# Optimization experiments

Hardware: AMD Instinct MI355X
Metric: run time of the kernel (lower is better)

Reference implementation:

```python
import jax, jax.numpy as jnp
import numpy as np

DIM = 2048
NUM_HEADS = 16
HEAD_DIM = DIM // NUM_HEADS  # 128
HIDDEN = HEAD_DIM * NUM_HEADS  # 2048


def setup_inputs() -> dict:
    key = jax.random.key(0)
    k1, k2, k3 = jax.random.split(key, 3)
    x = jax.random.normal(k1, (2, 4096, DIM), dtype=jnp.float32)
    # match torch init: gates.weight ~ N(0, dim**-0.5), output.weight ~ N(0, hidden**-0.5)
    Wg = jax.random.normal(k2, (NUM_HEADS + 3 * HIDDEN, DIM), dtype=jnp.float32) * DIM ** -0.5
    bg = jnp.zeros((NUM_HEADS + 3 * HIDDEN,), dtype=jnp.float32)
    Wo = jax.random.normal(k3, (DIM, HIDDEN), dtype=jnp.float32) * HIDDEN ** -0.5
    bo = jnp.zeros((DIM,), dtype=jnp.float32)
    return {"x": x, "Wg": Wg, "bg": bg, "Wo": Wo, "bo": bo}


def _combine(a, b):
    # linear recurrence c_t = f_t * c_{t-1} + u_t as an associative op
    fa, ua = a
    fb, ub = b
    return fa * fb, fb * ua + ub


def reference(x, Wg, bg, Wo, bo):
    # x: [B, T, dim]
    g = jnp.einsum('btd,gd->btg', x, Wg) + bg  # [B, T, H + 3*hidden]
    f = jax.nn.sigmoid(g[..., :NUM_HEADS])  # [B, T, H]
    i = jax.nn.sigmoid(g[..., NUM_HEADS:NUM_HEADS + HIDDEN])
    t = jnp.tanh(g[..., NUM_HEADS + HIDDEN:NUM_HEADS + 2 * HIDDEN])
    o = g[..., NUM_HEADS + 2 * HIDDEN:]
    f = jnp.repeat(f, HEAD_DIM, axis=-1)  # tied forget gate per head -> [B, T, hidden]
    update = i * t
    # scan over time axis (axis=1)
    _, c = jax.lax.associative_scan(_combine, (f, update), axis=1)
    h = o * jnp.tanh(c)
    return jnp.einsum('bth,dh->btd', h, Wo) + bo
```

## Files before the change

kernel.cpp:

```cpp
#include <hip/hip_runtime.h>
#include <hip/hip_bf16.h>

#define DIM 2048
#define NHEADS 16
#define HEAD_DIM 128
#define HIDDEN 2048
#define SEQ 4096
#define BATCH 2
#define BT (BATCH * SEQ)
#define NSEG 64
#define SEGLEN (SEQ / NSEG)
#define N_GATE (3 * HIDDEN)

typedef __bf16 bf16_t;
typedef __bf16 bf16x8 __attribute__((ext_vector_type(8)));
typedef __bf16 bf16x4_t __attribute__((ext_vector_type(4)));
typedef float f32x4 __attribute__((ext_vector_type(4)));

__device__ __forceinline__ void gload_lds16(const void* g, void* l) {
  __builtin_amdgcn_global_load_lds(
      (const __attribute__((address_space(1))) void*)g,
      (__attribute__((address_space(3))) void*)l, 16, 0, 0);
}

#define MEMFENCE asm volatile("" ::: "memory")
#define BAR do { MEMFENCE; __builtin_amdgcn_s_barrier(); MEMFENCE; } while (0)
#define VMCNT(n) asm volatile("s_waitcnt vmcnt(" #n ")" ::: "memory")

__global__ void cvt_f32_bf16(const float* __restrict__ src, bf16_t* __restrict__ dst, int n4) {
  int i = blockIdx.x * blockDim.x + threadIdx.x;
  if (i >= n4) return;
  float4 v = reinterpret_cast<const float4*>(src)[i];
  bf16x4_t o;
  o[0] = (bf16_t)v.x; o[1] = (bf16_t)v.y; o[2] = (bf16_t)v.z; o[3] = (bf16_t)v.w;
  reinterpret_cast<bf16x4_t*>(dst)[i] = o;
}

__global__ void fgate_kernel(const float* __restrict__ x, const float* __restrict__ Wg,
                             const float* __restrict__ bg, float* __restrict__ fout) {
  int idx = blockIdx.x * 256 + threadIdx.x;
  int bt = idx >> 4, h = idx & 15;
  const float* xr = x + (size_t)bt * DIM;
  const float* wr = Wg + (size_t)h * DIM;
  float acc = 0.f;
  for (int k = 0; k < DIM; k += 4) {
    float4 xv = *reinterpret_cast<const float4*>(xr + k);
    float4 wv = *reinterpret_cast<const float4*>(wr + k);
    acc = fmaf(xv.x, wv.x, acc);
    acc = fmaf(xv.y, wv.y, acc);
    acc = fmaf(xv.z, wv.z, acc);
    acc = fmaf(xv.w, wv.w, acc);
  }
  acc += bg[h];
  fout[idx] = 1.f / (1.f + expf(-acc));
}


__device__ __forceinline__ void stageA(const bf16_t* __restrict__ G, int brow, int kc,
                                       bf16_t* Aslot, int q, int wid, int lane) {
  const int rr = q * 64 + wid * 8;
  const int grow = brow + (wid >> 2) * 128 + q * 32 + (wid & 3) * 8 + (lane >> 3);
  const int gcol = kc + (((lane & 7) ^ (lane >> 3)) << 3);
  gload_lds16(G + (size_t)grow * 2048 + gcol, Aslot + (size_t)rr * 64);
}

__device__ __forceinline__ void stageB(const bf16_t* __restrict__ G, int bcol, int kc,
                                       bf16_t* Bslot, int j, int wid, int lane) {
  const int rr = (j >> 1) * 128 + (j & 1) * 64 + wid * 8;
  const int grow = bcol + rr + (lane >> 3);
  const int gcol = kc + (((lane & 7) ^ (lane >> 3)) << 3);
  gload_lds16(G + (size_t)grow * 2048 + gcol, Bslot + (size_t)rr * 64);
}

#define FRAG8(ptr, row, fo) (*reinterpret_cast<const bf16x8*>(&(ptr)[(size_t)(row) * 64 + (fo)]))

template <int MODE>
__global__ __launch_bounds__(512, 1)
void gemm256(const bf16_t* __restrict__ A, const bf16_t* __restrict__ B,
             const float* __restrict__ bias,
             bf16_t* __restrict__ Oi, bf16_t* __restrict__ Ot, bf16_t* __restrict__ Oo,
             float* __restrict__ Of, int tiles_n) {
  __shared__ __align__(16) bf16_t As[2][256 * 64];
  __shared__ __align__(16) bf16_t Bs[2][256 * 64];
  constexpr int KT = 32;

  const int tid = threadIdx.x;
  const int wid = tid >> 6, lane = tid & 63;
  const int nwg = gridDim.x, bid = blockIdx.x;
  const int swz = (bid & 7) * (nwg >> 3) + (bid >> 3);
  const int tm = swz / tiles_n, tn = swz - tm * tiles_n;
  const int brow = tm * 256, bcol = tn * 256;
  const int wm = wid >> 2, wn = wid & 3;
  const int rl = lane & 15, qw = lane >> 4;
  const int fo0 = ((qw ^ (rl & 7)) << 3);
  const int fo1 = fo0 ^ 32;
  const int brr = (wn >> 1) * 128 + (wn & 1) * 64;

  f32x4 acc[8][4] = {};

#pragma unroll
  for (int j = 0; j < 4; ++j) stageB(B, bcol, 0, &Bs[0][0], j, wid, lane);
#pragma unroll
  for (int qq = 0; qq < 4; ++qq) stageA(A, brow, 0, &As[0][0], qq, wid, lane);
#pragma unroll
  for (int qq = 0; qq < 3; ++qq) stageA(A, brow, 64, &As[1][0], qq, wid, lane);
  VMCNT(3);
  BAR;

  for (int t = 0; t < KT; ++t) {
    const int s = t & 1, ns = s ^ 1;
    const int kc1 = (t + 1) * 64, kc2 = (t + 2) * 64;
    const bool st1 = (t + 1) < KT, st2 = (t + 2) < KT;
    const bf16_t* Ar = &As[s][0];
    const bf16_t* Br = &Bs[s][0];
    bf16x8 bfr[2][4], af[2][2];

#define MFMA16(p)                                                                         \
  __builtin_amdgcn_s_setprio(1);                                                          \
  _Pragma("unroll")                                                                       \
  for (int mi = 0; mi < 2; ++mi)                                                          \
    _Pragma("unroll")                                                                     \
    for (int ni = 0; ni < 4; ++ni)                                                        \
      acc[(p)*2 + mi][ni] =                                                               \
          __builtin_amdgcn_mfma_f32_16x16x32_bf16(af[0][mi], bfr[0][ni], acc[(p)*2 + mi][ni], 0, 0, 0); \
  _Pragma("unroll")                                                                       \
  for (int mi = 0; mi < 2; ++mi)                                                          \
    _Pragma("unroll")                                                                     \
    for (int ni = 0; ni < 4; ++ni)                                                        \
      acc[(p)*2 + mi][ni] =                                                               \
          __builtin_amdgcn_mfma_f32_16x16x32_bf16(af[1][mi], bfr[1][ni], acc[(p)*2 + mi][ni], 0, 0, 0); \
  __builtin_amdgcn_s_setprio(0)

#pragma unroll
    for (int ni = 0; ni < 4; ++ni) {
      bfr[0][ni] = FRAG8(Br, brr + ni * 16 + rl, fo0);
      bfr[1][ni] = FRAG8(Br, brr + ni * 16 + rl, fo1);
    }
#pragma unroll
    for (int mi = 0; mi < 2; ++mi) {
      af[0][mi] = FRAG8(Ar, 0 * 64 + wm * 32 + mi * 16 + rl, fo0);
      af[1][mi] = FRAG8(Ar, 0 * 64 + wm * 32 + mi * 16 + rl, fo1);
    }
    if (st1) { stageB(B, bcol, kc1, &Bs[ns][0], 0, wid, lane);
               stageB(B, bcol, kc1, &Bs[ns][0], 1, wid, lane); }
    BAR;
    MFMA16(0);

#pragma unroll
    for (int mi = 0; mi < 2; ++mi) {
      af[0][mi] = FRAG8(Ar, 1 * 64 + wm * 32 + mi * 16 + rl, fo0);
      af[1][mi] = FRAG8(Ar, 1 * 64 + wm * 32 + mi * 16 + rl, fo1);
    }
    if (st1) { stageB(B, bcol, kc1, &Bs[ns][0], 2, wid, lane);
               stageB(B, bcol, kc1, &Bs[ns][0], 3, wid, lane); }
    if (t < KT - 1) { VMCNT(4); } else { VMCNT(0); }
    BAR;
    MFMA16(1);

#pragma unroll
    for (int mi = 0; mi < 2; ++mi) {
      af[0][mi] = FRAG8(Ar, 2 * 64 + wm * 32 + mi * 16 + rl, fo0);
      af[1][mi] = FRAG8(Ar, 2 * 64 + wm * 32 + mi * 16 + rl, fo1);
    }
    if (st2) { stageA(A, brow, kc2, &As[s][0], 0, wid, lane);
               stageA(A, brow, kc2, &As[s][0], 1, wid, lane); }
    BAR;
    MFMA16(2);

#pragma unroll
    for (int mi = 0; mi < 2; ++mi) {
      af[0][mi] = FRAG8(Ar, 3 * 64 + wm * 32 + mi * 16 + rl, fo0);
      af[1][mi] = FRAG8(Ar, 3 * 64 + wm * 32 + mi * 16 + rl, fo1);
    }
    if (st2) stageA(A, brow, kc2, &As[s][0], 2, wid, lane);
    if (st1) stageA(A, brow, kc1, &As[ns][0], 3, wid, lane);
    if (t < KT - 2) { VMCNT(4); }
    else if (t == KT - 2) { VMCNT(1); }
    BAR;
    MFMA16(3);
#undef MFMA16
  }

  const int crow0 = brow + wm * 128;
  const int ccol0 = bcol + wn * 64;
  if (MODE == 0) {
    const int section = bcol >> 11;
    bf16_t* dst = (section == 0) ? Oi : ((section == 1) ? Ot : Oo);
#pragma unroll
    for (int mi = 0; mi < 8; ++mi)
#pragma unroll
      for (int ni = 0; ni < 4; ++ni) {
        int gcol = ccol0 + ni * 16 + (lane & 15);
        int col = gcol & 2047;
        float bv = bias[gcol];
#pragma unroll
        for (int qq = 0; qq < 4; ++qq) {
          int row = crow0 + mi * 16 + (lane >> 4) * 4 + qq;
          float v = acc[mi][ni][qq] + bv;
          float aout;
          if (section == 0)      aout = 1.f / (1.f + __expf(-v));
          else if (section == 1) aout = tanhf(v);
          else                   aout = v;
          dst[(size_t)row * HIDDEN + col] = (bf16_t)aout;
        }
      }
  } else {
#pragma unroll
    for (int mi = 0; mi < 8; ++mi)
#pragma unroll
      for (int ni = 0; ni < 4; ++ni) {
        int col = ccol0 + ni * 16 + (lane & 15);
        float bv = bias[col];
#pragma unroll
        for (int qq = 0; qq < 4; ++qq) {
          int row = crow0 + mi * 16 + (lane >> 4) * 4 + qq;
          Of[(size_t)row * DIM + col] = acc[mi][ni][qq] + bv;
        }
      }
  }
}

__global__ void scan_pass1(const float* __restrict__ fg, const bf16_t* __restrict__ gi,
                           const bf16_t* __restrict__ gt, float* __restrict__ cend,
                           float* __restrict__ pseg) {
  int bx = blockIdx.x;
  int chblk = bx & 7, seg = (bx >> 3) & 63, b = bx >> 9;
  int ch = chblk * 256 + threadIdx.x;
  int head = ch >> 7;
  float c = 0.f, P = 1.f;
  size_t t0 = (size_t)b * SEQ + (size_t)seg * SEGLEN;
  for (int tt = 0; tt < SEGLEN; ++tt) {
    size_t bt = t0 + tt;
    float f = fg[bt * NHEADS + head];
    float iv = (float)gi[bt * HIDDEN + ch];
    float tv = (float)gt[bt * HIDDEN + ch];
    c = fmaf(f, c, iv * tv);
    P *= f;
  }
  size_t o = ((size_t)b * NSEG + seg) * HIDDEN + ch;
  cend[o] = c;
  pseg[o] = P;
}

__global__ void scan_pass2(const float* __restrict__ cend, const float* __restrict__ pseg,
                           float* __restrict__ cin) {
  int idx = blockIdx.x * 256 + threadIdx.x;
  int b = idx >> 11, ch = idx & 2047;
  float C = 0.f;
  for (int s = 0; s < NSEG; ++s) {
    size_t o = ((size_t)b * NSEG + s) * HIDDEN + ch;
    cin[o] = C;
    C = cend[o] + pseg[o] * C;
  }
}

__global__ void scan_pass3(const float* __restrict__ fg, const bf16_t* __restrict__ gi,
                           const bf16_t* __restrict__ gt, const bf16_t* __restrict__ go,
                           const float* __restrict__ cin, bf16_t* __restrict__ h) {
  int bx = blockIdx.x;
  int chblk = bx & 7, seg = (bx >> 3) & 63, b = bx >> 9;
  int ch = chblk * 256 + threadIdx.x;
  int head = ch >> 7;
  float c = cin[((size_t)b * NSEG + seg) * HIDDEN + ch];
  size_t t0 = (size_t)b * SEQ + (size_t)seg * SEGLEN;
  for (int tt = 0; tt < SEGLEN; ++tt) {
    size_t bt = t0 + tt;
    float f = fg[bt * NHEADS + head];
    float iv = (float)gi[bt * HIDDEN + ch];
    float tv = (float)gt[bt * HIDDEN + ch];
    c = fmaf(f, c, iv * tv);
    float hv = (float)go[bt * HIDDEN + ch] * tanhf(c);
    h[bt * HIDDEN + ch] = (bf16_t)hv;
  }
}

extern "C" void kernel_launch(void* const* d_in, const int* in_sizes, int n_in,
                              void* d_out, int out_size, void* d_ws, size_t ws_size,
                              hipStream_t stream) {
  const float* x  = (const float*)d_in[0];
  const float* Wg = (const float*)d_in[1];
  const float* bg = (const float*)d_in[2];
  const float* Wo = (const float*)d_in[3];
  const float* bo = (const float*)d_in[4];
  float* out = (float*)d_out;

  char* ws = (char*)d_ws;
  size_t off = 0;
  auto alloc = [&](size_t bytes) -> void* {
    void* p = ws + off;
    off += (bytes + 255) & ~(size_t)255;
    return p;
  };
  bf16_t* xb   = (bf16_t*)alloc((size_t)BT * DIM * 2);
  bf16_t* wgb  = (bf16_t*)alloc((size_t)N_GATE * DIM * 2);
  bf16_t* wob  = (bf16_t*)alloc((size_t)DIM * HIDDEN * 2);
  float*  fg   = (float*)alloc((size_t)BT * NHEADS * 4);
  bf16_t* gi   = (bf16_t*)alloc((size_t)BT * HIDDEN * 2);
  bf16_t* gt   = (bf16_t*)alloc((size_t)BT * HIDDEN * 2);
  bf16_t* go   = (bf16_t*)alloc((size_t)BT * HIDDEN * 2);
  bf16_t* hbuf = (bf16_t*)alloc((size_t)BT * HIDDEN * 2);
  float*  cend = (float*)alloc((size_t)BATCH * NSEG * HIDDEN * 4);
  float*  pseg = (float*)alloc((size_t)BATCH * NSEG * HIDDEN * 4);
  float*  cin  = (float*)alloc((size_t)BATCH * NSEG * HIDDEN * 4);
  (void)ws_size; (void)in_sizes; (void)n_in; (void)out_size;

  {
    int n4 = BT * DIM / 4;
    cvt_f32_bf16<<<(n4 + 255) / 256, 256, 0, stream>>>(x, xb, n4);
  }
  {
    int n4 = N_GATE * DIM / 4;
    cvt_f32_bf16<<<(n4 + 255) / 256, 256, 0, stream>>>(Wg + (size_t)NHEADS * DIM, wgb, n4);
  }
  {
    int n4 = DIM * HIDDEN / 4;
    cvt_f32_bf16<<<(n4 + 255) / 256, 256, 0, stream>>>(Wo, wob, n4);
  }

  fgate_kernel<<<(BT * NHEADS) / 256, 256, 0, stream>>>(x, Wg, bg, fg);

  gemm256<0><<<768, 512, 0, stream>>>(xb, wgb, bg + NHEADS, gi, gt, go, nullptr, 24);

  scan_pass1<<<BATCH * NSEG * (HIDDEN / 256), 256, 0, stream>>>(fg, gi, gt, cend, pseg);
  scan_pass2<<<BATCH * HIDDEN / 256, 256, 0, stream>>>(cend, pseg, cin);
  scan_pass3<<<BATCH * NSEG * (HIDDEN / 256), 256, 0, stream>>>(fg, gi, gt, go, cin, hbuf);

  gemm256<1><<<256, 512, 0, stream>>>(hbuf, wob, bo, nullptr, nullptr, nullptr, out, 8);
}
```

Measured before the change: 498.8 us.

## Use 4 waves per 256x256 GEMM tile with 128x128 per-wave subtiles

The 256x256 bf16 GEMM block drops from 8 waves to 4, and each wave now computes a 128x128 output subtile (8x8 MFMA fragments) instead of 128x64. This roughly doubles per-wave register reuse of A/B fragments from LDS and halves LDS read traffic per MFMA. Global-to-LDS staging is rewritten for 256 threads with more loads per thread and adjusted vmcnt waits. The cost is 256 accumulator registers per lane and less latency hiding from fewer waves per CU, which risks spills or stalls.

```diff
diff --git a/kernel.cpp b/kernel.cpp
--- a/kernel.cpp
+++ b/kernel.cpp
@@ -56,26 +56,18 @@
 }
 
 
-__device__ __forceinline__ void stageA(const bf16_t* __restrict__ G, int brow, int kc,
-                                       bf16_t* Aslot, int q, int wid, int lane) {
-  const int rr = q * 64 + wid * 8;
-  const int grow = brow + (wid >> 2) * 128 + q * 32 + (wid & 3) * 8 + (lane >> 3);
-  const int gcol = kc + (((lane & 7) ^ (lane >> 3)) << 3);
-  gload_lds16(G + (size_t)grow * 2048 + gcol, Aslot + (size_t)rr * 64);
-}
-
-__device__ __forceinline__ void stageB(const bf16_t* __restrict__ G, int bcol, int kc,
-                                       bf16_t* Bslot, int j, int wid, int lane) {
-  const int rr = (j >> 1) * 128 + (j & 1) * 64 + wid * 8;
-  const int grow = bcol + rr + (lane >> 3);
-  const int gcol = kc + (((lane & 7) ^ (lane >> 3)) << 3);
-  gload_lds16(G + (size_t)grow * 2048 + gcol, Bslot + (size_t)rr * 64);
+__device__ __forceinline__ void stage_u(const bf16_t* __restrict__ G, int grow0, int kc,
+                                        bf16_t* region, int u, int tid) {
+  const int row = u * 32 + (tid >> 3);
+  const int c = (tid & 7) ^ ((tid >> 3) & 7);
+  gload_lds16(G + (size_t)(grow0 + row) * 2048 + kc + c * 8,
+              region + (size_t)(u * 32 + (tid >> 6) * 8) * 64);
 }
 
 #define FRAG8(ptr, row, fo) (*reinterpret_cast<const bf16x8*>(&(ptr)[(size_t)(row) * 64 + (fo)]))
 
 template <int MODE>
-__global__ __launch_bounds__(512, 1)
+__global__ __launch_bounds__(256, 1)
 void gemm256(const bf16_t* __restrict__ A, const bf16_t* __restrict__ B,
              const float* __restrict__ bias,
              bf16_t* __restrict__ Oi, bf16_t* __restrict__ Ot, bf16_t* __restrict__ Oo,
@@ -90,21 +82,24 @@
   const int swz = (bid & 7) * (nwg >> 3) + (bid >> 3);
   const int tm = swz / tiles_n, tn = swz - tm * tiles_n;
   const int brow = tm * 256, bcol = tn * 256;
-  const int wm = wid >> 2, wn = wid & 3;
+  const int wm = wid >> 1, wn = wid & 1;
   const int rl = lane & 15, qw = lane >> 4;
   const int fo0 = ((qw ^ (rl & 7)) << 3);
   const int fo1 = fo0 ^ 32;
-  const int brr = (wn >> 1) * 128 + (wn & 1) * 64;
-
-  f32x4 acc[8][4] = {};
-
-#pragma unroll
-  for (int j = 0; j < 4; ++j) stageB(B, bcol, 0, &Bs[0][0], j, wid, lane);
-#pragma unroll
-  for (int qq = 0; qq < 4; ++qq) stageA(A, brow, 0, &As[0][0], qq, wid, lane);
-#pragma unroll
-  for (int qq = 0; qq < 3; ++qq) stageA(A, brow, 64, &As[1][0], qq, wid, lane);
-  VMCNT(3);
+
+  f32x4 acc[8][8] = {};
+
+#pragma unroll
+  for (int u = 0; u < 8; ++u) stage_u(B, bcol, 0, &Bs[0][0], u, tid);
+#pragma unroll
+  for (int u = 0; u < 8; ++u) stage_u(A, brow, 0, &As[0][0], u, tid);
+  stage_u(A, brow, 64, &As[1][0], 0, tid);
+  stage_u(A, brow, 64, &As[1][0], 1, tid);
+  stage_u(A, brow, 64, &As[1][0], 4, tid);
+  stage_u(A, brow, 64, &As[1][0], 5, tid);
+  stage_u(A, brow, 64, &As[1][0], 2, tid);
+  stage_u(A, brow, 64, &As[1][0], 6, tid);
+  VMCNT(6);
   BAR;
 
   for (int t = 0; t < KT; ++t) {
@@ -113,90 +108,100 @@
     const bool st1 = (t + 1) < KT, st2 = (t + 2) < KT;
     const bf16_t* Ar = &As[s][0];
     const bf16_t* Br = &Bs[s][0];
-    bf16x8 bfr[2][4], af[2][2];
-
-#define MFMA16(p)                                                                         \
+    bf16x8 bfr[2][8], af[2][2];
+
+#define MFMA32(p)                                                                         \
   __builtin_amdgcn_s_setprio(1);                                                          \
   _Pragma("unroll")                                                                       \
   for (int mi = 0; mi < 2; ++mi)                                                          \
     _Pragma("unroll")                                                                     \
-    for (int ni = 0; ni < 4; ++ni)                                                        \
-      acc[(p)*2 + mi][ni] =                                                               \
-          __builtin_amdgcn_mfma_f32_16x16x32_bf16(af[0][mi], bfr[0][ni], acc[(p)*2 + mi][ni], 0, 0, 0); \
+    for (int nj = 0; nj < 8; ++nj)                                                        \
+      acc[(p)*2 + mi][nj] =                                                               \
+          __builtin_amdgcn_mfma_f32_16x16x32_bf16(af[0][mi], bfr[0][nj], acc[(p)*2 + mi][nj], 0, 0, 0); \
   _Pragma("unroll")                                                                       \
   for (int mi = 0; mi < 2; ++mi)                                                          \
     _Pragma("unroll")                                                                     \
-    for (int ni = 0; ni < 4; ++ni)                                                        \
-      acc[(p)*2 + mi][ni] =                                                               \
-          __builtin_amdgcn_mfma_f32_16x16x32_bf16(af[1][mi], bfr[1][ni], acc[(p)*2 + mi][ni], 0, 0, 0); \
+    for (int nj = 0; nj < 8; ++nj)                                                        \
+      acc[(p)*2 + mi][nj] =                                                               \
+          __builtin_amdgcn_mfma_f32_16x16x32_bf16(af[1][mi], bfr[1][nj], acc[(p)*2 + mi][nj], 0, 0, 0); \
   __builtin_amdgcn_s_setprio(0)
 
 #pragma unroll
-    for (int ni = 0; ni < 4; ++ni) {
-      bfr[0][ni] = FRAG8(Br, brr + ni * 16 + rl, fo0);
-      bfr[1][ni] = FRAG8(Br, brr + ni * 16 + rl, fo1);
+    for (int nj = 0; nj < 8; ++nj) {
+      bfr[0][nj] = FRAG8(Br, wn * 128 + nj * 16 + rl, fo0);
+      bfr[1][nj] = FRAG8(Br, wn * 128 + nj * 16 + rl, fo1);
     }
 #pragma unroll
     for (int mi = 0; mi < 2; ++mi) {
-      af[0][mi] = FRAG8(Ar, 0 * 64 + wm * 32 + mi * 16 + rl, fo0);
-      af[1][mi] = FRAG8(Ar, 0 * 64 + wm * 32 + mi * 16 + rl, fo1);
-    }
-    if (st1) { stageB(B, bcol, kc1, &Bs[ns][0], 0, wid, lane);
-               stageB(B, bcol, kc1, &Bs[ns][0], 1, wid, lane); }
+      af[0][mi] = FRAG8(Ar, wm * 128 + 0 * 32 + mi * 16 + rl, fo0);
+      af[1][mi] = FRAG8(Ar, wm * 128 + 0 * 32 + mi * 16 + rl, fo1);
+    }
+    if (st1) {
+#pragma unroll
+      for (int u = 0; u < 4; ++u) stage_u(B, bcol, kc1, &Bs[ns][0], u, tid);
+    }
     BAR;
-    MFMA16(0);
+    MFMA32(0);
 
 #pragma unroll
     for (int mi = 0; mi < 2; ++mi) {
-      af[0][mi] = FRAG8(Ar, 1 * 64 + wm * 32 + mi * 16 + rl, fo0);
-      af[1][mi] = FRAG8(Ar, 1 * 64 + wm * 32 + mi * 16 + rl, fo1);
-    }
-    if (st1) { stageB(B, bcol, kc1, &Bs[ns][0], 2, wid, lane);
-               stageB(B, bcol, kc1, &Bs[ns][0], 3, wid, lane); }
-    if (t < KT - 1) { VMCNT(4); } else { VMCNT(0); }
+      af[0][mi] = FRAG8(Ar, wm * 128 + 1 * 32 + mi * 16 + rl, fo0);
+      af[1][mi] = FRAG8(Ar, wm * 128 + 1 * 32 + mi * 16 + rl, fo1);
+    }
+    if (st1) {
+#pragma unroll
+      for (int u = 4; u < 8; ++u) stage_u(B, bcol, kc1, &Bs[ns][0], u, tid);
+    }
+    if (t < KT - 1) { VMCNT(8); } else { VMCNT(0); }
     BAR;
-    MFMA16(1);
+    MFMA32(1);
 
 #pragma unroll
     for (int mi = 0; mi < 2; ++mi) {
-      af[0][mi] = FRAG8(Ar, 2 * 64 + wm * 32 + mi * 16 + rl, fo0);
-      af[1][mi] = FRAG8(Ar, 2 * 64 + wm * 32 + mi * 16 + rl, fo1);
-    }
-    if (st2) { stageA(A, brow, kc2, &As[s][0], 0, wid, lane);
-               stageA(A, brow, kc2, &As[s][0], 1, wid, lane); }
+      af[0][mi] = FRAG8(Ar, wm * 128 + 2 * 32 + mi * 16 + rl, fo0);
+      af[1][mi] = FRAG8(Ar, wm * 128 + 2 * 32 + mi * 16 + rl, fo1);
+    }
+    if (st2) {
+      stage_u(A, brow, kc2, &As[s][0], 0, tid);
+      stage_u(A, brow, kc2, &As[s][0], 1, tid);
+      stage_u(A, brow, kc2, &As[s][0], 4, tid);
+      stage_u(A, brow, kc2, &As[s][0], 5, tid);
+    }
     BAR;
-    MFMA16(2);
+    MFMA32(2);
 
 #pragma unroll
     for (int mi = 0; mi < 2; ++mi) {
-      af[0][mi] = FRAG8(Ar, 3 * 64 + wm * 32 + mi * 16 + rl, fo0);
-      af[1][mi] = FRAG8(Ar, 3 * 64 + wm * 32 + mi * 16 + rl, fo1);
-    }
-    if (st2) stageA(A, brow, kc2, &As[s][0], 2, wid, lane);
-    if (st1) stageA(A, brow, kc1, &As[ns][0], 3, wid, lane);
-    if (t < KT - 2) { VMCNT(4); }
-    else if (t == KT - 2) { VMCNT(1); }
+      af[0][mi] = FRAG8(Ar, wm * 128 + 3 * 32 + mi * 16 + rl, fo0);
+      af[1][mi] = FRAG8(Ar, wm * 128 + 3 * 32 + mi * 16 + rl, fo1);
+    }
+    if (st2) { stage_u(A, brow, kc2, &As[s][0], 2, tid);
+               stage_u(A, brow, kc2, &As[s][0], 6, tid); }
+    if (st1) { stage_u(A, brow, kc1, &As[ns][0], 3, tid);
+               stage_u(A, brow, kc1, &As[ns][0], 7, tid); }
+    if (t < KT - 2) { VMCNT(8); }
+    else if (t == KT - 2) { VMCNT(2); }
     BAR;
-    MFMA16(3);
-#undef MFMA16
+    MFMA32(3);
+#undef MFMA32
   }
 
   const int crow0 = brow + wm * 128;
-  const int ccol0 = bcol + wn * 64;
+  const int ccol0 = bcol + wn * 128;
   if (MODE == 0) {
     const int section = bcol >> 11;
     bf16_t* dst = (section == 0) ? Oi : ((section == 1) ? Ot : Oo);
 #pragma unroll
     for (int mi = 0; mi < 8; ++mi)
 #pragma unroll
-      for (int ni = 0; ni < 4; ++ni) {
-        int gcol = ccol0 + ni * 16 + (lane & 15);
+      for (int nj = 0; nj < 8; ++nj) {
+        int gcol = ccol0 + nj * 16 + rl;
         int col = gcol & 2047;
         float bv = bias[gcol];
 #pragma unroll
         for (int qq = 0; qq < 4; ++qq) {
-          int row = crow0 + mi * 16 + (lane >> 4) * 4 + qq;
-          float v = acc[mi][ni][qq] + bv;
+          int row = crow0 + mi * 16 + qw * 4 + qq;
+          float v = acc[mi][nj][qq] + bv;
           float aout;
           if (section == 0)      aout = 1.f / (1.f + __expf(-v));
           else if (section == 1) aout = tanhf(v);
@@ -208,13 +213,13 @@
 #pragma unroll
     for (int mi = 0; mi < 8; ++mi)
 #pragma unroll
-      for (int ni = 0; ni < 4; ++ni) {
-        int col = ccol0 + ni * 16 + (lane & 15);
+      for (int nj = 0; nj < 8; ++nj) {
+        int col = ccol0 + nj * 16 + rl;
         float bv = bias[col];
 #pragma unroll
         for (int qq = 0; qq < 4; ++qq) {
-          int row = crow0 + mi * 16 + (lane >> 4) * 4 + qq;
-          Of[(size_t)row * DIM + col] = acc[mi][ni][qq] + bv;
+          int row = crow0 + mi * 16 + qw * 4 + qq;
+          Of[(size_t)row * DIM + col] = acc[mi][nj][qq] + bv;
         }
       }
   }
@@ -319,11 +324,11 @@
 
   fgate_kernel<<<(BT * NHEADS) / 256, 256, 0, stream>>>(x, Wg, bg, fg);
 
-  gemm256<0><<<768, 512, 0, stream>>>(xb, wgb, bg + NHEADS, gi, gt, go, nullptr, 24);
+  gemm256<0><<<768, 256, 0, stream>>>(xb, wgb, bg + NHEADS, gi, gt, go, nullptr, 24);
 
   scan_pass1<<<BATCH * NSEG * (HIDDEN / 256), 256, 0, stream>>>(fg, gi, gt, cend, pseg);
   scan_pass2<<<BATCH * HIDDEN / 256, 256, 0, stream>>>(cend, pseg, cin);
   scan_pass3<<<BATCH * NSEG * (HIDDEN / 256), 256, 0, stream>>>(fg, gi, gt, go, cin, hbuf);
 
-  gemm256<1><<<256, 512, 0, stream>>>(hbuf, wob, bo, nullptr, nullptr, nullptr, out, 8);
-}
+  gemm256<1><<<256, 256, 0, stream>>>(hbuf, wob, bo, nullptr, nullptr, nullptr, out, 8);
+}
```

Measured after the change: 912.1 us. 1.83x slower.
